# Performance work log

Hardware: AMD Instinct MI355X
Metric: run time of the kernel (lower is better)

## Reference

```python
import jax, jax.numpy as jnp
import numpy as np

B, T, D, H, L = 8192, 512, 8, 64, 3  # batch, seq_len, input_size, hidden_size, num_layers


def setup_inputs() -> dict:
    key = jax.random.key(0)
    ks = iter(jax.random.split(key, 40))
    s = 1.0 / np.sqrt(H)
    inp = {
        "enc_x": jax.random.normal(next(ks), (B, T, D), jnp.float32),
        "dec_x": jax.random.normal(next(ks), (B, T, D), jnp.float32),
    }
    for pfx, in0 in (("enc", D), ("dec", D + H)):  # decoder layer0 sees cat([x, y_t_1])
        for l in range(L):
            fan = in0 if l == 0 else H
            inp[f"{pfx}_Wih{l}"] = s * jax.random.normal(next(ks), (4 * H, fan), jnp.float32)
            inp[f"{pfx}_Whh{l}"] = s * jax.random.normal(next(ks), (4 * H, H), jnp.float32)
            inp[f"{pfx}_b{l}"] = s * jax.random.normal(next(ks), (4 * H,), jnp.float32)  # b_ih + b_hh fused
    inp["fc_W"] = s * jax.random.normal(next(ks), (D, H), jnp.float32)
    inp["fc_b"] = jnp.zeros((D,), jnp.float32)
    return inp


def _cell(x, h, c, Wih, Whh, b):
    # PyTorch LSTM gate order: i, f, g, o
    g = x @ Wih.T + h @ Whh.T + b
    i, f, gg, o = jnp.split(g, 4, axis=-1)
    c = jax.nn.sigmoid(f) * c + jax.nn.sigmoid(i) * jnp.tanh(gg)
    h = jax.nn.sigmoid(o) * jnp.tanh(c)
    return h, c


def _stack(x_t, hs, cs, params):
    inp, nh, nc = x_t, [], []
    for l, (Wih, Whh, b) in enumerate(params):
        h, c = _cell(inp, hs[l], cs[l], Wih, Whh, b)
        nh.append(h); nc.append(c); inp = h
    return tuple(nh), tuple(nc)


def reference(enc_x, dec_x,
              enc_Wih0, enc_Whh0, enc_b0, enc_Wih1, enc_Whh1, enc_b1, enc_Wih2, enc_Whh2, enc_b2,
              dec_Wih0, dec_Whh0, dec_b0, dec_Wih1, dec_Whh1, dec_b1, dec_Wih2, dec_Whh2, dec_b2,
              fc_W, fc_b):
    enc_params = [(enc_Wih0, enc_Whh0, enc_b0), (enc_Wih1, enc_Whh1, enc_b1), (enc_Wih2, enc_Whh2, enc_b2)]
    dec_params = [(dec_Wih0, dec_Whh0, dec_b0), (dec_Wih1, dec_Whh1, dec_b1), (dec_Wih2, dec_Whh2, dec_b2)]
    b = enc_x.shape[0]
    hd = enc_Whh0.shape[1]
    nl = len(enc_params)
    zeros = tuple(jnp.zeros((b, hd), enc_x.dtype) for _ in range(nl))

    # ----- encoder: run LSTM over enc_x, keep only final (h, c) -----
    def enc_step(carry, x_t):
        hs, cs = carry
        return _stack(x_t, hs, cs, enc_params), None

    (hs, cs), _ = jax.lax.scan(enc_step, (zeros, zeros), jnp.swapaxes(enc_x, 0, 1))

    # ----- decoder: per-timestep, input = cat([dec_x_t, y_{t-1}]) -----
    def dec_step(carry, x_t):
        y_prev, hs, cs = carry
        inp = jnp.concatenate([x_t, y_prev], axis=-1)
        hs, cs = _stack(inp, hs, cs, dec_params)
        y_t = hs[-1]
        pred = y_t @ fc_W.T + fc_b
        return (y_t, hs, cs), pred

    y0 = jnp.zeros((b, hd), enc_x.dtype)
    _, preds = jax.lax.scan(dec_step, (y0, hs, cs), jnp.swapaxes(dec_x, 0, 1))
    return jnp.swapaxes(preds, 0, 1)  # (B, T, D)
```

## Files before the change

### kernel.cpp

```cpp
#include <hip/hip_runtime.h>


#define TT   512
#define DD   8
#define HH   64
#define MM   32
#define S0   168
#define S12  136
#define NP   260

typedef _Float16 half8  __attribute__((ext_vector_type(8)));
typedef _Float16 half4  __attribute__((ext_vector_type(4)));
typedef float    floatx4 __attribute__((ext_vector_type(4)));

__device__ __forceinline__ float sigf(float x) {
    return __builtin_amdgcn_rcpf(1.0f + __expf(-x));
}
__device__ __forceinline__ float tanhfast(float x) {
    return 1.0f - 2.0f * __builtin_amdgcn_rcpf(1.0f + __expf(2.0f * x));
}

__device__ __forceinline__ half8 ldfrag_l12(const float* Wih, const float* Whh,
                                            int n, int s) {
    const float* src = (s < HH) ? (Wih + n * HH + s) : (Whh + n * HH + (s - HH));
    half8 r;
#pragma unroll
    for (int j = 0; j < 8; ++j) r[j] = (_Float16)src[j];
    return r;
}

__device__ __forceinline__ half8 ldfrag_l0(const float* Wih, int kih,
                                           const float* Whh, int n, int s) {
    half8 r;
    const float* src = nullptr;
    if (s < 8)        src = Wih + n * kih + s;
    else if (s < 32)  src = nullptr;
    else if (s < 96)  src = Whh + n * HH + (s - 32);
    else              src = Wih + n * kih + (s - 88);
    if (src) {
#pragma unroll
        for (int j = 0; j < 8; ++j) r[j] = (_Float16)src[j];
    } else {
#pragma unroll
        for (int j = 0; j < 8; ++j) r[j] = (_Float16)0.f;
    }
    return r;
}

template <int KT, int KW>
__device__ __forceinline__ void gemm_layer(const _Float16* panel, int stride,
                                           const half8 (&wf)[KW][2],
                                           const float (&br)[2], float* gb,
                                           int l15, int q, int nbase) {
    floatx4 acc[2][2];
#pragma unroll
    for (int mt = 0; mt < 2; ++mt)
#pragma unroll
        for (int nt = 0; nt < 2; ++nt)
            acc[mt][nt] = (floatx4){br[nt], br[nt], br[nt], br[nt]};
#pragma unroll
    for (int kt = 0; kt < KT; ++kt) {
        const _Float16* pk = panel + kt * 32 + q * 8;
        half8 a0 = *(const half8*)(pk + l15 * stride);
        half8 a1 = *(const half8*)(pk + (16 + l15) * stride);
        acc[0][0] = __builtin_amdgcn_mfma_f32_16x16x32_f16(a0, wf[kt][0], acc[0][0], 0, 0, 0);
        acc[0][1] = __builtin_amdgcn_mfma_f32_16x16x32_f16(a0, wf[kt][1], acc[0][1], 0, 0, 0);
        acc[1][0] = __builtin_amdgcn_mfma_f32_16x16x32_f16(a1, wf[kt][0], acc[1][0], 0, 0, 0);
        acc[1][1] = __builtin_amdgcn_mfma_f32_16x16x32_f16(a1, wf[kt][1], acc[1][1], 0, 0, 0);
    }
#pragma unroll
    for (int mt = 0; mt < 2; ++mt)
#pragma unroll
        for (int nt = 0; nt < 2; ++nt) {
            const int n = nbase + nt * 16 + l15;
#pragma unroll
            for (int r = 0; r < 4; ++r)
                gb[(mt * 16 + q * 4 + r) * NP + n] = acc[mt][nt][r];
        }
}

__device__ __forceinline__ void ew_layer(const float* g, float (&c)[4],
                                         _Float16* h0dst, _Float16* h1dst) {
    floatx4 gi = *(const floatx4*)(g);
    floatx4 gf = *(const floatx4*)(g + 64);
    floatx4 gg = *(const floatx4*)(g + 128);
    floatx4 go = *(const floatx4*)(g + 192);
    half4 h4;
#pragma unroll
    for (int j = 0; j < 4; ++j) {
        float iv = sigf(gi[j]);
        float fv = sigf(gf[j]);
        float gv = tanhfast(gg[j]);
        float ov = sigf(go[j]);
        float cv = fv * c[j] + iv * gv;
        c[j] = cv;
        h4[j] = (_Float16)(ov * tanhfast(cv));
    }
    *(half4*)h0dst = h4;
    if (h1dst) *(half4*)h1dst = h4;
}

__global__ __launch_bounds__(512, 2) void seq2seq_kernel(
    const float* __restrict__ encx, const float* __restrict__ decx,
    const float* __restrict__ eW0i, const float* __restrict__ eW0h, const float* __restrict__ eb0,
    const float* __restrict__ eW1i, const float* __restrict__ eW1h, const float* __restrict__ eb1,
    const float* __restrict__ eW2i, const float* __restrict__ eW2h, const float* __restrict__ eb2,
    const float* __restrict__ dW0i, const float* __restrict__ dW0h, const float* __restrict__ db0,
    const float* __restrict__ dW1i, const float* __restrict__ dW1h, const float* __restrict__ db1,
    const float* __restrict__ dW2i, const float* __restrict__ dW2h, const float* __restrict__ db2,
    const float* __restrict__ fcW, const float* __restrict__ fcb,
    float* __restrict__ out) {
    __shared__ _Float16 p0[MM * S0];
    __shared__ _Float16 p1[MM * S12];
    __shared__ _Float16 p2[MM * S12];
    __shared__ float gbuf[MM * NP];

    const int tid  = threadIdx.x;
    const int lane = tid & 63;
    const int wave = tid >> 6;
    const int l15  = lane & 15;
    const int q    = lane >> 4;
    const int nbase = wave * 32;
    const int rbase = blockIdx.x * MM;

    const int em = tid >> 4;
    const int eu = (tid & 15) * 4;

    for (int i = tid; i < MM * S0; i += 512)  p0[i] = (_Float16)0.f;
    for (int i = tid; i < MM * S12; i += 512) p1[i] = (_Float16)0.f;
    for (int i = tid; i < MM * S12; i += 512) p2[i] = (_Float16)0.f;

    float c0[4] = {0, 0, 0, 0}, c1[4] = {0, 0, 0, 0}, c2[4] = {0, 0, 0, 0};

    half8 w0[5][2], w1[4][2], w2[4][2];
    float b0r[2], b1r[2], b2r[2];
#pragma unroll
    for (int nt = 0; nt < 2; ++nt) {
        const int n = nbase + nt * 16 + l15;
#pragma unroll
        for (int kt = 0; kt < 3; ++kt) w0[kt][nt] = ldfrag_l0(eW0i, 8, eW0h, n, kt * 32 + q * 8);
#pragma unroll
        for (int kt = 0; kt < 4; ++kt) w1[kt][nt] = ldfrag_l12(eW1i, eW1h, n, kt * 32 + q * 8);
#pragma unroll
        for (int kt = 0; kt < 4; ++kt) w2[kt][nt] = ldfrag_l12(eW2i, eW2h, n, kt * 32 + q * 8);
        b0r[nt] = eb0[n]; b1r[nt] = eb1[n]; b2r[nt] = eb2[n];
    }

    const int xrow = tid >> 3;
    const int xcol = tid & 7;
    float xr = 0.f;
    if (tid < 256) xr = encx[(size_t)(rbase + xrow) * TT * DD + xcol];

    _Float16* h0w = p0 + em * S0 + 32 + eu;
    _Float16* x1w = p1 + em * S12 + eu;
    _Float16* h1w = p1 + em * S12 + 64 + eu;
    _Float16* x2w = p2 + em * S12 + eu;
    _Float16* h2w = p2 + em * S12 + 64 + eu;
    _Float16* yw  = p0 + em * S0 + 96 + eu;
    float* gme = gbuf + em * NP + eu;

    __syncthreads();

    for (int t = 0; t < TT; ++t) {
        if (tid < 256) p0[xrow * S0 + xcol] = (_Float16)xr;
        __syncthreads();
        if (tid < 256 && t + 1 < TT)
            xr = encx[(size_t)(rbase + xrow) * TT * DD + (t + 1) * DD + xcol];
        gemm_layer<3>(p0, S0, w0, b0r, gbuf, l15, q, nbase);
        __syncthreads();
        ew_layer(gme, c0, h0w, x1w);
        __syncthreads();
        gemm_layer<4>(p1, S12, w1, b1r, gbuf, l15, q, nbase);
        __syncthreads();
        ew_layer(gme, c1, h1w, x2w);
        __syncthreads();
        gemm_layer<4>(p2, S12, w2, b2r, gbuf, l15, q, nbase);
        __syncthreads();
        ew_layer(gme, c2, h2w, nullptr);
    }

    __syncthreads();

#pragma unroll
    for (int nt = 0; nt < 2; ++nt) {
        const int n = nbase + nt * 16 + l15;
#pragma unroll
        for (int kt = 0; kt < 5; ++kt) w0[kt][nt] = ldfrag_l0(dW0i, 72, dW0h, n, kt * 32 + q * 8);
#pragma unroll
        for (int kt = 0; kt < 4; ++kt) w1[kt][nt] = ldfrag_l12(dW1i, dW1h, n, kt * 32 + q * 8);
#pragma unroll
        for (int kt = 0; kt < 4; ++kt) w2[kt][nt] = ldfrag_l12(dW2i, dW2h, n, kt * 32 + q * 8);
        b0r[nt] = db0[n]; b1r[nt] = db1[n]; b2r[nt] = db2[n];
    }
    half8 fw[2];
    const float fbr = (l15 < 8) ? fcb[l15] : 0.f;
#pragma unroll
    for (int kt = 0; kt < 2; ++kt) {
        half8 r;
        if (l15 < 8) {
            const float* s = fcW + l15 * HH + kt * 32 + q * 8;
#pragma unroll
            for (int j = 0; j < 8; ++j) r[j] = (_Float16)s[j];
        } else {
#pragma unroll
            for (int j = 0; j < 8; ++j) r[j] = (_Float16)0.f;
        }
        fw[kt] = r;
    }

    *(half4*)yw = (half4){(_Float16)0.f, (_Float16)0.f, (_Float16)0.f, (_Float16)0.f};
    if (tid < 256) xr = decx[(size_t)(rbase + xrow) * TT * DD + xcol];

    for (int t = 0; t < TT; ++t) {
        if (tid < 256) p0[xrow * S0 + xcol] = (_Float16)xr;
        __syncthreads();
        if (tid < 256 && t + 1 < TT)
            xr = decx[(size_t)(rbase + xrow) * TT * DD + (t + 1) * DD + xcol];
        gemm_layer<5>(p0, S0, w0, b0r, gbuf, l15, q, nbase);
        __syncthreads();
        ew_layer(gme, c0, h0w, x1w);
        __syncthreads();
        gemm_layer<4>(p1, S12, w1, b1r, gbuf, l15, q, nbase);
        __syncthreads();
        ew_layer(gme, c1, h1w, x2w);
        __syncthreads();
        gemm_layer<4>(p2, S12, w2, b2r, gbuf, l15, q, nbase);
        __syncthreads();
        ew_layer(gme, c2, h2w, yw);
        __syncthreads();
        if (wave == 0 || wave == 4) {
            const int mt = wave >> 2;
            floatx4 fa = (floatx4){fbr, fbr, fbr, fbr};
#pragma unroll
            for (int kt = 0; kt < 2; ++kt) {
                half8 a = *(const half8*)(p2 + (mt * 16 + l15) * S12 + 64 + kt * 32 + q * 8);
                fa = __builtin_amdgcn_mfma_f32_16x16x32_f16(a, fw[kt], fa, 0, 0, 0);
            }
            if (l15 < 8) {
#pragma unroll
                for (int r = 0; r < 4; ++r)
                    out[(size_t)(rbase + mt * 16 + q * 4 + r) * TT * DD + (size_t)t * DD + l15] = fa[r];
            }
        }
    }
}

extern "C" void kernel_launch(void* const* d_in, const int* in_sizes, int n_in,
                              void* d_out, int out_size, void* d_ws, size_t ws_size,
                              hipStream_t stream) {
    const float* encx = (const float*)d_in[0];
    const float* decx = (const float*)d_in[1];
    const float* eW0i = (const float*)d_in[2];
    const float* eW0h = (const float*)d_in[3];
    const float* eb0  = (const float*)d_in[4];
    const float* eW1i = (const float*)d_in[5];
    const float* eW1h = (const float*)d_in[6];
    const float* eb1  = (const float*)d_in[7];
    const float* eW2i = (const float*)d_in[8];
    const float* eW2h = (const float*)d_in[9];
    const float* eb2  = (const float*)d_in[10];
    const float* dW0i = (const float*)d_in[11];
    const float* dW0h = (const float*)d_in[12];
    const float* db0  = (const float*)d_in[13];
    const float* dW1i = (const float*)d_in[14];
    const float* dW1h = (const float*)d_in[15];
    const float* db1  = (const float*)d_in[16];
    const float* dW2i = (const float*)d_in[17];
    const float* dW2h = (const float*)d_in[18];
    const float* db2  = (const float*)d_in[19];
    const float* fcW  = (const float*)d_in[20];
    const float* fcb  = (const float*)d_in[21];
    float* out = (float*)d_out;

    seq2seq_kernel<<<dim3(256), dim3(512), 0, stream>>>(
        encx, decx, eW0i, eW0h, eb0, eW1i, eW1h, eb1, eW2i, eW2h, eb2,
        dW0i, dW0h, db0, dW1i, dW1h, db1, dW2i, dW2h, db2, fcW, fcb, out);
}
```

Before: 3.676 ms.

## Halve rows per block to launch 512 blocks and fill all CUs

Reduces the batch rows handled per block from 32 to 16, which doubles the grid to 512 blocks, and raises the launch-bounds occupancy hint to 4 blocks per CU. The GEMM now issues one M-tile of MFMAs per wave instead of two, and each elementwise thread handles 2 hidden units instead of 4. The aim is to spread the serial recurrence over more CUs (256 blocks would leave many of the MI355X's CUs idle), shortening each block's critical path per timestep. In exchange, every block repeats the weight loads and barrier overhead for half as much work, and MFMA utilisation per wave falls.

```diff
diff --git a/kernel.cpp b/kernel.cpp
--- a/kernel.cpp
+++ b/kernel.cpp
@@ -4,14 +4,15 @@
 #define TT   512
 #define DD   8
 #define HH   64
-#define MM   32
+#define MM   16
 #define S0   168
 #define S12  136
 #define NP   260
 
 typedef _Float16 half8  __attribute__((ext_vector_type(8)));
-typedef _Float16 half4  __attribute__((ext_vector_type(4)));
+typedef _Float16 half2t __attribute__((ext_vector_type(2)));
 typedef float    floatx4 __attribute__((ext_vector_type(4)));
+typedef float    floatx2 __attribute__((ext_vector_type(2)));
 
 __device__ __forceinline__ float sigf(float x) {
     return __builtin_amdgcn_rcpf(1.0f + __expf(-x));
@@ -52,55 +53,47 @@
                                            const half8 (&wf)[KW][2],
                                            const float (&br)[2], float* gb,
                                            int l15, int q, int nbase) {
-    floatx4 acc[2][2];
-#pragma unroll
-    for (int mt = 0; mt < 2; ++mt)
-#pragma unroll
-        for (int nt = 0; nt < 2; ++nt)
-            acc[mt][nt] = (floatx4){br[nt], br[nt], br[nt], br[nt]};
+    floatx4 acc[2];
+#pragma unroll
+    for (int nt = 0; nt < 2; ++nt)
+        acc[nt] = (floatx4){br[nt], br[nt], br[nt], br[nt]};
 #pragma unroll
     for (int kt = 0; kt < KT; ++kt) {
-        const _Float16* pk = panel + kt * 32 + q * 8;
-        half8 a0 = *(const half8*)(pk + l15 * stride);
-        half8 a1 = *(const half8*)(pk + (16 + l15) * stride);
-        acc[0][0] = __builtin_amdgcn_mfma_f32_16x16x32_f16(a0, wf[kt][0], acc[0][0], 0, 0, 0);
-        acc[0][1] = __builtin_amdgcn_mfma_f32_16x16x32_f16(a0, wf[kt][1], acc[0][1], 0, 0, 0);
-        acc[1][0] = __builtin_amdgcn_mfma_f32_16x16x32_f16(a1, wf[kt][0], acc[1][0], 0, 0, 0);
-        acc[1][1] = __builtin_amdgcn_mfma_f32_16x16x32_f16(a1, wf[kt][1], acc[1][1], 0, 0, 0);
-    }
-#pragma unroll
-    for (int mt = 0; mt < 2; ++mt)
-#pragma unroll
-        for (int nt = 0; nt < 2; ++nt) {
-            const int n = nbase + nt * 16 + l15;
-#pragma unroll
-            for (int r = 0; r < 4; ++r)
-                gb[(mt * 16 + q * 4 + r) * NP + n] = acc[mt][nt][r];
-        }
-}
-
-__device__ __forceinline__ void ew_layer(const float* g, float (&c)[4],
+        half8 a0 = *(const half8*)(panel + l15 * stride + kt * 32 + q * 8);
+        acc[0] = __builtin_amdgcn_mfma_f32_16x16x32_f16(a0, wf[kt][0], acc[0], 0, 0, 0);
+        acc[1] = __builtin_amdgcn_mfma_f32_16x16x32_f16(a0, wf[kt][1], acc[1], 0, 0, 0);
+    }
+#pragma unroll
+    for (int nt = 0; nt < 2; ++nt) {
+        const int n = nbase + nt * 16 + l15;
+#pragma unroll
+        for (int r = 0; r < 4; ++r)
+            gb[(q * 4 + r) * NP + n] = acc[nt][r];
+    }
+}
+
+__device__ __forceinline__ void ew_layer(const float* g, float (&c)[2],
                                          _Float16* h0dst, _Float16* h1dst) {
-    floatx4 gi = *(const floatx4*)(g);
-    floatx4 gf = *(const floatx4*)(g + 64);
-    floatx4 gg = *(const floatx4*)(g + 128);
-    floatx4 go = *(const floatx4*)(g + 192);
-    half4 h4;
-#pragma unroll
-    for (int j = 0; j < 4; ++j) {
+    floatx2 gi = *(const floatx2*)(g);
+    floatx2 gf = *(const floatx2*)(g + 64);
+    floatx2 gg = *(const floatx2*)(g + 128);
+    floatx2 go = *(const floatx2*)(g + 192);
+    half2t h2;
+#pragma unroll
+    for (int j = 0; j < 2; ++j) {
         float iv = sigf(gi[j]);
         float fv = sigf(gf[j]);
         float gv = tanhfast(gg[j]);
         float ov = sigf(go[j]);
         float cv = fv * c[j] + iv * gv;
         c[j] = cv;
-        h4[j] = (_Float16)(ov * tanhfast(cv));
-    }
-    *(half4*)h0dst = h4;
-    if (h1dst) *(half4*)h1dst = h4;
-}
-
-__global__ __launch_bounds__(512, 2) void seq2seq_kernel(
+        h2[j] = (_Float16)(ov * tanhfast(cv));
+    }
+    *(half2t*)h0dst = h2;
+    if (h1dst) *(half2t*)h1dst = h2;
+}
+
+__global__ __launch_bounds__(512, 4) void seq2seq_kernel(
     const float* __restrict__ encx, const float* __restrict__ decx,
     const float* __restrict__ eW0i, const float* __restrict__ eW0h, const float* __restrict__ eb0,
     const float* __restrict__ eW1i, const float* __restrict__ eW1h, const float* __restrict__ eb1,
@@ -123,14 +116,14 @@
     const int nbase = wave * 32;
     const int rbase = blockIdx.x * MM;
 
-    const int em = tid >> 4;
-    const int eu = (tid & 15) * 4;
+    const int em = tid >> 5;
+    const int eu = (tid & 31) * 2;
 
     for (int i = tid; i < MM * S0; i += 512)  p0[i] = (_Float16)0.f;
     for (int i = tid; i < MM * S12; i += 512) p1[i] = (_Float16)0.f;
     for (int i = tid; i < MM * S12; i += 512) p2[i] = (_Float16)0.f;
 
-    float c0[4] = {0, 0, 0, 0}, c1[4] = {0, 0, 0, 0}, c2[4] = {0, 0, 0, 0};
+    float c0[2] = {0, 0}, c1[2] = {0, 0}, c2[2] = {0, 0};
 
     half8 w0[5][2], w1[4][2], w2[4][2];
     float b0r[2], b1r[2], b2r[2];
@@ -149,7 +142,7 @@
     const int xrow = tid >> 3;
     const int xcol = tid & 7;
     float xr = 0.f;
-    if (tid < 256) xr = encx[(size_t)(rbase + xrow) * TT * DD + xcol];
+    if (tid < 128) xr = encx[(size_t)(rbase + xrow) * TT * DD + xcol];
 
     _Float16* h0w = p0 + em * S0 + 32 + eu;
     _Float16* x1w = p1 + em * S12 + eu;
@@ -162,9 +155,9 @@
     __syncthreads();
 
     for (int t = 0; t < TT; ++t) {
-        if (tid < 256) p0[xrow * S0 + xcol] = (_Float16)xr;
-        __syncthreads();
-        if (tid < 256 && t + 1 < TT)
+        if (tid < 128) p0[xrow * S0 + xcol] = (_Float16)xr;
+        __syncthreads();
+        if (tid < 128 && t + 1 < TT)
             xr = encx[(size_t)(rbase + xrow) * TT * DD + (t + 1) * DD + xcol];
         gemm_layer<3>(p0, S0, w0, b0r, gbuf, l15, q, nbase);
         __syncthreads();
@@ -208,13 +201,13 @@
         fw[kt] = r;
     }
 
-    *(half4*)yw = (half4){(_Float16)0.f, (_Float16)0.f, (_Float16)0.f, (_Float16)0.f};
-    if (tid < 256) xr = decx[(size_t)(rbase + xrow) * TT * DD + xcol];
+    *(half2t*)yw = (half2t){(_Float16)0.f, (_Float16)0.f};
+    if (tid < 128) xr = decx[(size_t)(rbase + xrow) * TT * DD + xcol];
 
     for (int t = 0; t < TT; ++t) {
-        if (tid < 256) p0[xrow * S0 + xcol] = (_Float16)xr;
-        __syncthreads();
-        if (tid < 256 && t + 1 < TT)
+        if (tid < 128) p0[xrow * S0 + xcol] = (_Float16)xr;
+        __syncthreads();
+        if (tid < 128 && t + 1 < TT)
             xr = decx[(size_t)(rbase + xrow) * TT * DD + (t + 1) * DD + xcol];
         gemm_layer<5>(p0, S0, w0, b0r, gbuf, l15, q, nbase);
         __syncthreads();
@@ -228,18 +221,17 @@
         __syncthreads();
         ew_layer(gme, c2, h2w, yw);
         __syncthreads();
-        if (wave == 0 || wave == 4) {
-            const int mt = wave >> 2;
+        if (wave == 0) {
             floatx4 fa = (floatx4){fbr, fbr, fbr, fbr};
 #pragma unroll
             for (int kt = 0; kt < 2; ++kt) {
-                half8 a = *(const half8*)(p2 + (mt * 16 + l15) * S12 + 64 + kt * 32 + q * 8);
+                half8 a = *(const half8*)(p2 + l15 * S12 + 64 + kt * 32 + q * 8);
                 fa = __builtin_amdgcn_mfma_f32_16x16x32_f16(a, fw[kt], fa, 0, 0, 0);
             }
             if (l15 < 8) {
 #pragma unroll
                 for (int r = 0; r < 4; ++r)
-                    out[(size_t)(rbase + mt * 16 + q * 4 + r) * TT * DD + (size_t)t * DD + l15] = fa[r];
+                    out[(size_t)(rbase + q * 4 + r) * TT * DD + (size_t)t * DD + l15] = fa[r];
             }
         }
     }
@@ -272,7 +264,7 @@
     const float* fcb  = (const float*)d_in[21];
     float* out = (float*)d_out;
 
-    seq2seq_kernel<<<dim3(256), dim3(512), 0, stream>>>(
+    seq2seq_kernel<<<dim3(512), dim3(512), 0, stream>>>(
         encx, decx, eW0i, eW0h, eb0, eW1i, eW1h, eb1, eW2i, eW2h, eb2,
         dW0i, dW0h, db0, dW1i, dW1h, db1, dW2i, dW2h, db2, fcW, fcb, out);
 }
```

After: 6.345 ms. +72.6%, slower.

## Permute gate columns per wave and double-buffer hidden state to cut barriers

Applied to the files above, without the earlier changes.

Reorders the weight columns so each wave owns all four gates (i,f,g,o) for 8 hidden units. The gate pre-activations can then stay in a per-wave LDS strip and the elementwise update runs without a block-wide barrier after each GEMM. Hidden states are double-buffered by timestep parity, which removes the read/write hazards and the barriers that guarded them. The FC output projection is deferred by one step and overlapped with the next step's layer-0 work. In exchange, panel strides grow and launch bounds drop to one block per CU, which risks lower occupancy and extra LDS use.

```diff
diff --git a/kernel.cpp b/kernel.cpp
--- a/kernel.cpp
+++ b/kernel.cpp
@@ -5,12 +5,12 @@
 #define DD   8
 #define HH   64
 #define MM   32
-#define S0   168
-#define S12  136
-#define NP   260
+#define S0   232
+#define S12  200
+#define WBS  36
+#define WSTRIP (32 * WBS)
 
 typedef _Float16 half8  __attribute__((ext_vector_type(8)));
-typedef _Float16 half4  __attribute__((ext_vector_type(4)));
 typedef float    floatx4 __attribute__((ext_vector_type(4)));
 
 __device__ __forceinline__ float sigf(float x) {
@@ -49,9 +49,10 @@
 
 template <int KT, int KW>
 __device__ __forceinline__ void gemm_layer(const _Float16* panel, int stride,
+                                           const int (&aoff)[KT],
                                            const half8 (&wf)[KW][2],
-                                           const float (&br)[2], float* gb,
-                                           int l15, int q, int nbase) {
+                                           const float (&br)[2],
+                                           float* wb, int l15, int q) {
     floatx4 acc[2][2];
 #pragma unroll
     for (int mt = 0; mt < 2; ++mt)
@@ -60,7 +61,7 @@
             acc[mt][nt] = (floatx4){br[nt], br[nt], br[nt], br[nt]};
 #pragma unroll
     for (int kt = 0; kt < KT; ++kt) {
-        const _Float16* pk = panel + kt * 32 + q * 8;
+        const _Float16* pk = panel + aoff[kt] + q * 8;
         half8 a0 = *(const half8*)(pk + l15 * stride);
         half8 a1 = *(const half8*)(pk + (16 + l15) * stride);
         acc[0][0] = __builtin_amdgcn_mfma_f32_16x16x32_f16(a0, wf[kt][0], acc[0][0], 0, 0, 0);
@@ -69,38 +70,42 @@
         acc[1][1] = __builtin_amdgcn_mfma_f32_16x16x32_f16(a1, wf[kt][1], acc[1][1], 0, 0, 0);
     }
 #pragma unroll
-    for (int mt = 0; mt < 2; ++mt)
-#pragma unroll
-        for (int nt = 0; nt < 2; ++nt) {
-            const int n = nbase + nt * 16 + l15;
+    for (int nt = 0; nt < 2; ++nt)
+#pragma unroll
+        for (int mt = 0; mt < 2; ++mt)
 #pragma unroll
             for (int r = 0; r < 4; ++r)
-                gb[(mt * 16 + q * 4 + r) * NP + n] = acc[mt][nt][r];
-        }
-}
-
-__device__ __forceinline__ void ew_layer(const float* g, float (&c)[4],
-                                         _Float16* h0dst, _Float16* h1dst) {
-    floatx4 gi = *(const floatx4*)(g);
-    floatx4 gf = *(const floatx4*)(g + 64);
-    floatx4 gg = *(const floatx4*)(g + 128);
-    floatx4 go = *(const floatx4*)(g + 192);
-    half4 h4;
+                wb[(mt * 16 + q * 4 + r) * WBS + nt * 16 + l15] = acc[mt][nt][r];
+}
+
+__device__ __forceinline__ void ew_layer(const float* wbr, int la7, float (&c)[4],
+                                         _Float16* pA, int sA, int offA,
+                                         _Float16* pB, int sB, int offB,
+                                         int uu, bool loLane) {
 #pragma unroll
     for (int j = 0; j < 4; ++j) {
-        float iv = sigf(gi[j]);
-        float fv = sigf(gf[j]);
-        float gv = tanhfast(gg[j]);
-        float ov = sigf(go[j]);
+        const int row = 8 * j + la7;
+        floatx4 g = *(const floatx4*)(wbr + row * WBS);
+        float iv = sigf(g[0]);
+        float fv = sigf(g[1]);
+        float gv = tanhfast(g[2]);
+        float ov = sigf(g[3]);
         float cv = fv * c[j] + iv * gv;
         c[j] = cv;
-        h4[j] = (_Float16)(ov * tanhfast(cv));
-    }
-    *(half4*)h0dst = h4;
-    if (h1dst) *(half4*)h1dst = h4;
-}
-
-__global__ __launch_bounds__(512, 2) void seq2seq_kernel(
+        _Float16 hv = (_Float16)(ov * tanhfast(cv));
+        unsigned short hb;
+        __builtin_memcpy(&hb, &hv, 2);
+        unsigned int mine = hb;
+        unsigned int oth = (unsigned int)__shfl_xor((int)mine, 8, 64);
+        if (loLane) {
+            unsigned int word = mine | (oth << 16);
+            *(unsigned int*)(pA + row * sA + offA + uu) = word;
+            if (pB) *(unsigned int*)(pB + row * sB + offB + uu) = word;
+        }
+    }
+}
+
+__global__ __launch_bounds__(512, 1) void seq2seq_kernel(
     const float* __restrict__ encx, const float* __restrict__ decx,
     const float* __restrict__ eW0i, const float* __restrict__ eW0h, const float* __restrict__ eb0,
     const float* __restrict__ eW1i, const float* __restrict__ eW1h, const float* __restrict__ eb1,
@@ -113,20 +118,22 @@
     __shared__ _Float16 p0[MM * S0];
     __shared__ _Float16 p1[MM * S12];
     __shared__ _Float16 p2[MM * S12];
-    __shared__ float gbuf[MM * NP];
+    __shared__ float wavebuf[8 * WSTRIP];
 
     const int tid  = threadIdx.x;
     const int lane = tid & 63;
     const int wave = tid >> 6;
     const int l15  = lane & 15;
     const int q    = lane >> 4;
-    const int nbase = wave * 32;
     const int rbase = blockIdx.x * MM;
 
-    const int em = tid >> 4;
-    const int eu = (tid & 15) * 4;
-
-    for (int i = tid; i < MM * S0; i += 512)  p0[i] = (_Float16)0.f;
+    const int la7 = lane & 7;
+    const int uu  = (wave << 3) + (lane >> 3);
+    const bool loLane = (((lane >> 3) & 1) == 0);
+    float* wb  = wavebuf + wave * WSTRIP;
+    const float* wbr = wb + (lane >> 3) * 4;
+
+    for (int i = tid; i < MM * S0;  i += 512) p0[i] = (_Float16)0.f;
     for (int i = tid; i < MM * S12; i += 512) p1[i] = (_Float16)0.f;
     for (int i = tid; i < MM * S12; i += 512) p2[i] = (_Float16)0.f;
 
@@ -136,7 +143,8 @@
     float b0r[2], b1r[2], b2r[2];
 #pragma unroll
     for (int nt = 0; nt < 2; ++nt) {
-        const int n = nbase + nt * 16 + l15;
+        const int cc = nt * 16 + l15;
+        const int n = (cc & 3) * 64 + (wave << 3) + (cc >> 2);
 #pragma unroll
         for (int kt = 0; kt < 3; ++kt) w0[kt][nt] = ldfrag_l0(eW0i, 8, eW0h, n, kt * 32 + q * 8);
 #pragma unroll
@@ -151,39 +159,41 @@
     float xr = 0.f;
     if (tid < 256) xr = encx[(size_t)(rbase + xrow) * TT * DD + xcol];
 
-    _Float16* h0w = p0 + em * S0 + 32 + eu;
-    _Float16* x1w = p1 + em * S12 + eu;
-    _Float16* h1w = p1 + em * S12 + 64 + eu;
-    _Float16* x2w = p2 + em * S12 + eu;
-    _Float16* h2w = p2 + em * S12 + 64 + eu;
-    _Float16* yw  = p0 + em * S0 + 96 + eu;
-    float* gme = gbuf + em * NP + eu;
-
     __syncthreads();
 
     for (int t = 0; t < TT; ++t) {
+        const int wp = t & 1;
+        const int rp = 1 - wp;
         if (tid < 256) p0[xrow * S0 + xcol] = (_Float16)xr;
         __syncthreads();
         if (tid < 256 && t + 1 < TT)
             xr = encx[(size_t)(rbase + xrow) * TT * DD + (t + 1) * DD + xcol];
-        gemm_layer<3>(p0, S0, w0, b0r, gbuf, l15, q, nbase);
-        __syncthreads();
-        ew_layer(gme, c0, h0w, x1w);
-        __syncthreads();
-        gemm_layer<4>(p1, S12, w1, b1r, gbuf, l15, q, nbase);
-        __syncthreads();
-        ew_layer(gme, c1, h1w, x2w);
-        __syncthreads();
-        gemm_layer<4>(p2, S12, w2, b2r, gbuf, l15, q, nbase);
-        __syncthreads();
-        ew_layer(gme, c2, h2w, nullptr);
+
+        {
+            const int aoff[3] = {0, 32 + 64 * rp, 64 + 64 * rp};
+            gemm_layer<3>(p0, S0, aoff, w0, b0r, wb, l15, q);
+            ew_layer(wbr, la7, c0, p0, S0, 32 + 64 * wp, p1, S12, 0, uu, loLane);
+        }
+        __syncthreads();
+        {
+            const int aoff[4] = {0, 32, 64 + 64 * rp, 96 + 64 * rp};
+            gemm_layer<4>(p1, S12, aoff, w1, b1r, wb, l15, q);
+            ew_layer(wbr, la7, c1, p1, S12, 64 + 64 * wp, p2, S12, 0, uu, loLane);
+        }
+        __syncthreads();
+        {
+            const int aoff[4] = {0, 32, 64 + 64 * rp, 96 + 64 * rp};
+            gemm_layer<4>(p2, S12, aoff, w2, b2r, wb, l15, q);
+            ew_layer(wbr, la7, c2, p2, S12, 64 + 64 * wp, (_Float16*)nullptr, 0, 0, uu, loLane);
+        }
     }
 
     __syncthreads();
 
 #pragma unroll
     for (int nt = 0; nt < 2; ++nt) {
-        const int n = nbase + nt * 16 + l15;
+        const int cc = nt * 16 + l15;
+        const int n = (cc & 3) * 64 + (wave << 3) + (cc >> 2);
 #pragma unroll
         for (int kt = 0; kt < 5; ++kt) w0[kt][nt] = ldfrag_l0(dW0i, 72, dW0h, n, kt * 32 + q * 8);
 #pragma unroll
@@ -208,39 +218,62 @@
         fw[kt] = r;
     }
 
-    *(half4*)yw = (half4){(_Float16)0.f, (_Float16)0.f, (_Float16)0.f, (_Float16)0.f};
     if (tid < 256) xr = decx[(size_t)(rbase + xrow) * TT * DD + xcol];
 
     for (int t = 0; t < TT; ++t) {
+        const int wp = t & 1;
+        const int rp = 1 - wp;
         if (tid < 256) p0[xrow * S0 + xcol] = (_Float16)xr;
         __syncthreads();
         if (tid < 256 && t + 1 < TT)
             xr = decx[(size_t)(rbase + xrow) * TT * DD + (t + 1) * DD + xcol];
-        gemm_layer<5>(p0, S0, w0, b0r, gbuf, l15, q, nbase);
-        __syncthreads();
-        ew_layer(gme, c0, h0w, x1w);
-        __syncthreads();
-        gemm_layer<4>(p1, S12, w1, b1r, gbuf, l15, q, nbase);
-        __syncthreads();
-        ew_layer(gme, c1, h1w, x2w);
-        __syncthreads();
-        gemm_layer<4>(p2, S12, w2, b2r, gbuf, l15, q, nbase);
-        __syncthreads();
-        ew_layer(gme, c2, h2w, yw);
-        __syncthreads();
-        if (wave == 0 || wave == 4) {
-            const int mt = wave >> 2;
-            floatx4 fa = (floatx4){fbr, fbr, fbr, fbr};
-#pragma unroll
-            for (int kt = 0; kt < 2; ++kt) {
-                half8 a = *(const half8*)(p2 + (mt * 16 + l15) * S12 + 64 + kt * 32 + q * 8);
-                fa = __builtin_amdgcn_mfma_f32_16x16x32_f16(a, fw[kt], fa, 0, 0, 0);
+
+        {
+            if (t > 0 && wave < 2) {
+                const int fp = 1 - wp;
+                floatx4 fa = (floatx4){fbr, fbr, fbr, fbr};
+#pragma unroll
+                for (int kt = 0; kt < 2; ++kt) {
+                    half8 a = *(const half8*)(p2 + (wave * 16 + l15) * S12 + 64 + 64 * fp + kt * 32 + q * 8);
+                    fa = __builtin_amdgcn_mfma_f32_16x16x32_f16(a, fw[kt], fa, 0, 0, 0);
+                }
+                if (l15 < 8) {
+#pragma unroll
+                    for (int r = 0; r < 4; ++r)
+                        out[(size_t)(rbase + wave * 16 + q * 4 + r) * TT * DD + (size_t)(t - 1) * DD + l15] = fa[r];
+                }
             }
-            if (l15 < 8) {
-#pragma unroll
-                for (int r = 0; r < 4; ++r)
-                    out[(size_t)(rbase + mt * 16 + q * 4 + r) * TT * DD + (size_t)t * DD + l15] = fa[r];
-            }
+            const int aoff[5] = {0, 32 + 64 * rp, 64 + 64 * rp, 160, 192};
+            gemm_layer<5>(p0, S0, aoff, w0, b0r, wb, l15, q);
+            ew_layer(wbr, la7, c0, p0, S0, 32 + 64 * wp, p1, S12, 0, uu, loLane);
+        }
+        __syncthreads();
+        {
+            const int aoff[4] = {0, 32, 64 + 64 * rp, 96 + 64 * rp};
+            gemm_layer<4>(p1, S12, aoff, w1, b1r, wb, l15, q);
+            ew_layer(wbr, la7, c1, p1, S12, 64 + 64 * wp, p2, S12, 0, uu, loLane);
+        }
+        __syncthreads();
+        {
+            const int aoff[4] = {0, 32, 64 + 64 * rp, 96 + 64 * rp};
+            gemm_layer<4>(p2, S12, aoff, w2, b2r, wb, l15, q);
+            ew_layer(wbr, la7, c2, p2, S12, 64 + 64 * wp, p0, S0, 160, uu, loLane);
+        }
+    }
+
+    __syncthreads();
+    if (wave < 2) {
+        const int fp = (TT - 1) & 1;
+        floatx4 fa = (floatx4){fbr, fbr, fbr, fbr};
+#pragma unroll
+        for (int kt = 0; kt < 2; ++kt) {
+            half8 a = *(const half8*)(p2 + (wave * 16 + l15) * S12 + 64 + 64 * fp + kt * 32 + q * 8);
+            fa = __builtin_amdgcn_mfma_f32_16x16x32_f16(a, fw[kt], fa, 0, 0, 0);
+        }
+        if (l15 < 8) {
+#pragma unroll
+            for (int r = 0; r < 4; ++r)
+                out[(size_t)(rbase + wave * 16 + q * 4 + r) * TT * DD + (size_t)(TT - 1) * DD + l15] = fa[r];
         }
     }
 }
```

Result: slower. 4.021 ms (+9.4%).
